# Optimization experiments

Hardware: AMD Instinct MI355X
Metric: run time of the kernel (lower is better)

## Reference

```python
import jax, jax.numpy as jnp
import numpy as np

B, LQ, LK, E, H = 2, 1024, 10000, 256, 8
D = E // H  # head_dim = 32


def setup_inputs() -> dict:
    key = jax.random.key(0)
    ks = jax.random.split(key, 10)
    s = 1.0 / np.sqrt(E).astype(np.float32)
    return {
        "bev_emb": jax.random.normal(ks[0], (B, LK, E), jnp.float32),
        "queries": jax.random.normal(ks[1], (B, LQ, E), jnp.float32),
        "Wq": jax.random.normal(ks[2], (E, E), jnp.float32) * s,
        "bq": jax.random.normal(ks[3], (E,), jnp.float32) * 0.01,
        "Wk": jax.random.normal(ks[4], (E, E), jnp.float32) * s,
        "bk": jax.random.normal(ks[5], (E,), jnp.float32) * 0.01,
        "Wv": jax.random.normal(ks[6], (E, E), jnp.float32) * s,
        "bv": jax.random.normal(ks[7], (E,), jnp.float32) * 0.01,
        "Wo": jax.random.normal(ks[8], (E, E), jnp.float32) * s,
        "bo": jax.random.normal(ks[9], (E,), jnp.float32) * 0.01,
    }


def reference(bev_emb, queries, Wq, bq, Wk, bk, Wv, bv, Wo, bo):
    Bn, Lq, Em = queries.shape
    Lk = bev_emb.shape[1]
    q = (queries @ Wq + bq).reshape(Bn, Lq, H, D)
    k = (bev_emb @ Wk + bk).reshape(Bn, Lk, H, D)
    v = (bev_emb @ Wv + bv).reshape(Bn, Lk, H, D)
    # NOTE: source applies no 1/sqrt(head_dim) scaling
    energy = jnp.einsum('bqhd,bkhd->bhqk', q, k)  # [B,H,Lq,Lk]
    attn = jax.nn.softmax(energy, axis=-1)
    out = jnp.einsum('bhqk,bkhd->bqhd', attn, v).reshape(Bn, Lq, Em)
    return out @ Wo + bo
```

## Files before the change

kernel.cpp:

```cpp
#include <hip/hip_runtime.h>
#include <hip/hip_bf16.h>

#define B_  2
#define LQ_ 1024
#define LK_ 10000
#define E_  256
#define H_  8
#define D_  32
#define NT_ ((LK_ + 63) / 64)
#define KVBLKS_ 625
#define QBLKS_  64

typedef __attribute__((ext_vector_type(8))) short bf16x8;
typedef __attribute__((ext_vector_type(4))) short bf16x4;
typedef __attribute__((ext_vector_type(4))) float f32x4;

#define LOG2E 1.4426950408889634f

static __device__ __forceinline__ short bfc(float x) {
  __bf16 b = (__bf16)x;
  return __builtin_bit_cast(short, b);
}
static __device__ __forceinline__ float bf2f(short s) {
  return (float)__builtin_bit_cast(__bf16, s);
}

#if __has_builtin(__builtin_amdgcn_exp2f)
static __device__ __forceinline__ float ex2(float x) {
  return __builtin_amdgcn_exp2f(x);
}
#else
static __device__ __forceinline__ float ex2(float x) { return exp2f(x); }
#endif

#if __has_builtin(__builtin_amdgcn_mfma_f32_16x16x16bf16_1k)
static __device__ __forceinline__ f32x4 mfma_pv(bf16x4 a, bf16x4 b, f32x4 c) {
  return __builtin_amdgcn_mfma_f32_16x16x16bf16_1k(a, b, c, 0, 0, 0);
}
#else
static __device__ __forceinline__ f32x4 mfma_pv(bf16x4 a, bf16x4 b, f32x4 c) {
  asm volatile("s_nop 1\n\tv_mfma_f32_16x16x16_bf16 %0, %1, %2, %0"
               : "+v"(c) : "v"(a), "v"(b));
  return c;
}
#endif

static __device__ __forceinline__ void tile_barrier() {
  __builtin_amdgcn_sched_barrier(0);
  asm volatile("s_waitcnt lgkmcnt(0)" ::: "memory");
  __builtin_amdgcn_s_barrier();
  __builtin_amdgcn_sched_barrier(0);
}

static __device__ __forceinline__ int xcd_swizzle(int flat, int nwg) {
  const int xcd = flat & 7, rest = flat >> 3;
  const int q = nwg >> 3, r = nwg & 7;
  return (xcd < r ? xcd * (q + 1) : r * (q + 1) + (xcd - r) * q) + rest;
}

static __device__ __forceinline__ void split8(const float4& a, const float4& b,
                                              bf16x8& hi, bf16x8& lo) {
  float v[8] = {a.x, a.y, a.z, a.w, b.x, b.y, b.z, b.w};
#pragma unroll
  for (int i = 0; i < 8; ++i) {
    const short h = bfc(v[i]);
    hi[i] = h;
    lo[i] = bfc(v[i] - bf2f(h));
  }
}

__global__ __launch_bounds__(256) void wtrans4(
    const float* __restrict__ W0, const float* __restrict__ W1,
    const float* __restrict__ W2, const float* __restrict__ W3,
    unsigned short* __restrict__ T0, unsigned short* __restrict__ T1,
    unsigned short* __restrict__ T2, unsigned short* __restrict__ T3) {
  const float* W;
  unsigned short* T;
  switch (blockIdx.z) {
    case 0:  W = W0; T = T0; break;
    case 1:  W = W1; T = T1; break;
    case 2:  W = W2; T = T2; break;
    default: W = W3; T = T3; break;
  }
  __shared__ float ts[16][17];
  const int tx = threadIdx.x & 15;
  const int ty = threadIdx.x >> 4;
  const int k0 = blockIdx.x * 16;
  const int n0 = blockIdx.y * 16;
  ts[ty][tx] = W[(size_t)(k0 + ty) * 256 + n0 + tx];
  __syncthreads();
  T[(size_t)(n0 + ty) * 256 + k0 + tx] = (unsigned short)bfc(ts[tx][ty]);
}

__global__ __launch_bounds__(256) void proj_all(
    const float* __restrict__ bev, const float* __restrict__ queries,
    const unsigned short* __restrict__ Wtk, const unsigned short* __restrict__ Wtv,
    const unsigned short* __restrict__ Wtq,
    const float* __restrict__ bk, const float* __restrict__ bv,
    const float* __restrict__ bq,
    unsigned short* __restrict__ kout, unsigned short* __restrict__ vout,
    float* __restrict__ qout) {
  const int lane = threadIdx.x & 63;
  const int nt   = threadIdx.x >> 6;
  const int lr   = lane & 15;
  const int oc   = lane >> 4;
  const int n0   = nt * 64;

  const bool isQ = (blockIdx.x >= KVBLKS_);
  const int  m0  = (isQ ? (int)blockIdx.x - KVBLKS_ : (int)blockIdx.x) * 32;
  const float* A = isQ ? queries : bev;
  const unsigned short* W1 = isQ ? Wtq : Wtk;

  f32x4 ac1[2][4], ac2[2][4];
#pragma unroll
  for (int s = 0; s < 2; ++s)
#pragma unroll
    for (int q = 0; q < 4; ++q) {
      ac1[s][q] = (f32x4){0.f, 0.f, 0.f, 0.f};
      ac2[s][q] = (f32x4){0.f, 0.f, 0.f, 0.f};
    }

  const float* a0p = &A[(size_t)(m0 + lr) * 256 + oc * 8];
  const float* a1p = a0p + 16 * 256;

  float4 ab[2][4];
  ab[0][0] = *(const float4*)(a0p + 0);
  ab[0][1] = *(const float4*)(a0p + 4);
  ab[0][2] = *(const float4*)(a1p + 0);
  ab[0][3] = *(const float4*)(a1p + 4);
  ab[1][0] = *(const float4*)(a0p + 32);
  ab[1][1] = *(const float4*)(a0p + 36);
  ab[1][2] = *(const float4*)(a1p + 32);
  ab[1][3] = *(const float4*)(a1p + 36);

#pragma unroll
  for (int kb = 0; kb < 8; ++kb) {
    const int bk_ = kb & 1;

    const int wko = kb * 32 + oc * 8;
    bf16x8 w1[4], w2[4];
#pragma unroll
    for (int q = 0; q < 4; ++q) {
      w1[q] = *(const bf16x8*)&W1[(size_t)(n0 + q * 16 + lr) * 256 + wko];
      if (!isQ) w2[q] = *(const bf16x8*)&Wtv[(size_t)(n0 + q * 16 + lr) * 256 + wko];
    }

    bf16x8 ah0, al0, ah1, al1;
    split8(ab[bk_][0], ab[bk_][1], ah0, al0);
    split8(ab[bk_][2], ab[bk_][3], ah1, al1);

    if (kb < 6) {
      ab[bk_][0] = *(const float4*)(a0p + (kb + 2) * 32 + 0);
      ab[bk_][1] = *(const float4*)(a0p + (kb + 2) * 32 + 4);
      ab[bk_][2] = *(const float4*)(a1p + (kb + 2) * 32 + 0);
      ab[bk_][3] = *(const float4*)(a1p + (kb + 2) * 32 + 4);
    }

#pragma unroll
    for (int q = 0; q < 4; ++q) {
      ac1[0][q] = __builtin_amdgcn_mfma_f32_16x16x32_bf16(w1[q], ah0, ac1[0][q], 0, 0, 0);
      ac1[0][q] = __builtin_amdgcn_mfma_f32_16x16x32_bf16(w1[q], al0, ac1[0][q], 0, 0, 0);
      ac1[1][q] = __builtin_amdgcn_mfma_f32_16x16x32_bf16(w1[q], ah1, ac1[1][q], 0, 0, 0);
      ac1[1][q] = __builtin_amdgcn_mfma_f32_16x16x32_bf16(w1[q], al1, ac1[1][q], 0, 0, 0);
      if (!isQ) {
        ac2[0][q] = __builtin_amdgcn_mfma_f32_16x16x32_bf16(w2[q], ah0, ac2[0][q], 0, 0, 0);
        ac2[1][q] = __builtin_amdgcn_mfma_f32_16x16x32_bf16(w2[q], ah1, ac2[1][q], 0, 0, 0);
      }
    }
  }

#pragma unroll
  for (int s = 0; s < 2; ++s) {
#pragma unroll
    for (int q = 0; q < 4; ++q) {
      const int m = m0 + s * 16 + lr;
      const int n = n0 + q * 16 + oc * 4;
      if (isQ) {
        const float4 b4 = *(const float4*)&bq[n];
        float4 o;
        o.x = ac1[s][q][0] + b4.x; o.y = ac1[s][q][1] + b4.y;
        o.z = ac1[s][q][2] + b4.z; o.w = ac1[s][q][3] + b4.w;
        *(float4*)&qout[(size_t)m * 256 + n] = o;
      } else {
        const float4 bk4 = *(const float4*)&bk[n];
        const float4 bv4 = *(const float4*)&bv[n];
        ushort4 ok, ov;
        ok.x = (unsigned short)bfc(ac1[s][q][0] + bk4.x);
        ok.y = (unsigned short)bfc(ac1[s][q][1] + bk4.y);
        ok.z = (unsigned short)bfc(ac1[s][q][2] + bk4.z);
        ok.w = (unsigned short)bfc(ac1[s][q][3] + bk4.w);
        ov.x = (unsigned short)bfc(ac2[s][q][0] + bv4.x);
        ov.y = (unsigned short)bfc(ac2[s][q][1] + bv4.y);
        ov.z = (unsigned short)bfc(ac2[s][q][2] + bv4.z);
        ov.w = (unsigned short)bfc(ac2[s][q][3] + bv4.w);
        *(ushort4*)&kout[(size_t)m * 256 + n] = ok;
        *(ushort4*)&vout[(size_t)m * 256 + n] = ov;
      }
    }
  }
}

__global__ __launch_bounds__(256) void proj_o(const float* __restrict__ A,
                                              const unsigned short* __restrict__ Wt,
                                              const float* __restrict__ bias,
                                              float* __restrict__ C) {
  const int lane = threadIdx.x & 63;
  const int nt   = threadIdx.x >> 6;
  const int lr   = lane & 15;
  const int oc   = lane >> 4;
  const int n0   = nt * 64;
  const int m0   = blockIdx.x * 32;

  f32x4 acc[2][4];
#pragma unroll
  for (int s = 0; s < 2; ++s)
#pragma unroll
    for (int q = 0; q < 4; ++q) acc[s][q] = (f32x4){0.f, 0.f, 0.f, 0.f};

  const float* a0p = &A[(size_t)(m0 + lr) * 256 + oc * 8];
  const float* a1p = a0p + 16 * 256;

  float4 ab[2][4];
  ab[0][0] = *(const float4*)(a0p + 0);
  ab[0][1] = *(const float4*)(a0p + 4);
  ab[0][2] = *(const float4*)(a1p + 0);
  ab[0][3] = *(const float4*)(a1p + 4);
  ab[1][0] = *(const float4*)(a0p + 32);
  ab[1][1] = *(const float4*)(a0p + 36);
  ab[1][2] = *(const float4*)(a1p + 32);
  ab[1][3] = *(const float4*)(a1p + 36);

#pragma unroll
  for (int kb = 0; kb < 8; ++kb) {
    const int bk_ = kb & 1;
    const int wko = kb * 32 + oc * 8;
    bf16x8 w[4];
#pragma unroll
    for (int q = 0; q < 4; ++q)
      w[q] = *(const bf16x8*)&Wt[(size_t)(n0 + q * 16 + lr) * 256 + wko];

    bf16x8 ah0, al0, ah1, al1;
    split8(ab[bk_][0], ab[bk_][1], ah0, al0);
    split8(ab[bk_][2], ab[bk_][3], ah1, al1);

    if (kb < 6) {
      ab[bk_][0] = *(const float4*)(a0p + (kb + 2) * 32 + 0);
      ab[bk_][1] = *(const float4*)(a0p + (kb + 2) * 32 + 4);
      ab[bk_][2] = *(const float4*)(a1p + (kb + 2) * 32 + 0);
      ab[bk_][3] = *(const float4*)(a1p + (kb + 2) * 32 + 4);
    }

#pragma unroll
    for (int q = 0; q < 4; ++q) {
      acc[0][q] = __builtin_amdgcn_mfma_f32_16x16x32_bf16(w[q], ah0, acc[0][q], 0, 0, 0);
      acc[0][q] = __builtin_amdgcn_mfma_f32_16x16x32_bf16(w[q], al0, acc[0][q], 0, 0, 0);
      acc[1][q] = __builtin_amdgcn_mfma_f32_16x16x32_bf16(w[q], ah1, acc[1][q], 0, 0, 0);
      acc[1][q] = __builtin_amdgcn_mfma_f32_16x16x32_bf16(w[q], al1, acc[1][q], 0, 0, 0);
    }
  }

#pragma unroll
  for (int s = 0; s < 2; ++s) {
#pragma unroll
    for (int q = 0; q < 4; ++q) {
      const int m = m0 + s * 16 + lr;
      const int n = n0 + q * 16 + oc * 4;
      const float4 b4 = *(const float4*)&bias[n];
      float4 o;
      o.x = acc[s][q][0] + b4.x; o.y = acc[s][q][1] + b4.y;
      o.z = acc[s][q][2] + b4.z; o.w = acc[s][q][3] + b4.w;
      *(float4*)&C[(size_t)m * 256 + n] = o;
    }
  }
}

__global__ __launch_bounds__(256, 4) void attn_mfma(const float* __restrict__ q,
                                                    const unsigned short* __restrict__ kbf,
                                                    const unsigned short* __restrict__ vbf,
                                                    float* __restrict__ Opart,
                                                    float* __restrict__ lpart,
                                                    float* __restrict__ o_direct,
                                                    int tiles_per_split, int nsplit) {
  const int nwg = 64 * gridDim.z;
  const int l   = xcd_swizzle(blockIdx.x + 8 * (blockIdx.y + 8 * blockIdx.z), nwg);
  const int qb   = l & 7;
  const int h    = (l >> 3) & 7;
  const int z    = l >> 6;
  const int s_id = z / B_;
  const int b    = z % B_;
  const int t    = threadIdx.x;
  const int lane = t & 63;
  const int w    = t >> 6;
  const int lq   = lane & 15;
  const int grp  = lane >> 4;

  __shared__ ushort Klds[2][64][64];
  __shared__ ushort Vtld[2][32][64];

  const int t0 = s_id * tiles_per_split;
  const int t1 = min(NT_, t0 + tiles_per_split);

  const int qrowA = qb * 128 + w * 32 + lq;
  const int qrowB = qrowA + 16;
  bf16x8 qfA, qfB;
  {
    const float* qpA = &q[((size_t)(b * LQ_ + qrowA)) * E_ + h * D_ + grp * 8];
    const float* qpB = &q[((size_t)(b * LQ_ + qrowB)) * E_ + h * D_ + grp * 8];
    const float4 a0 = *(const float4*)qpA;
    const float4 a1 = *(const float4*)(qpA + 4);
    const float4 b0 = *(const float4*)qpB;
    const float4 b1 = *(const float4*)(qpB + 4);
    qfA[0] = bfc(a0.x * LOG2E); qfA[1] = bfc(a0.y * LOG2E);
    qfA[2] = bfc(a0.z * LOG2E); qfA[3] = bfc(a0.w * LOG2E);
    qfA[4] = bfc(a1.x * LOG2E); qfA[5] = bfc(a1.y * LOG2E);
    qfA[6] = bfc(a1.z * LOG2E); qfA[7] = bfc(a1.w * LOG2E);
    qfB[0] = bfc(b0.x * LOG2E); qfB[1] = bfc(b0.y * LOG2E);
    qfB[2] = bfc(b0.z * LOG2E); qfB[3] = bfc(b0.w * LOG2E);
    qfB[4] = bfc(b1.x * LOG2E); qfB[5] = bfc(b1.y * LOG2E);
    qfB[6] = bfc(b1.z * LOG2E); qfB[7] = bfc(b1.w * LOG2E);
  }

  const int krow_l = t >> 2;
  const int kchunk = t & 3;
  const int vkp    = t >> 3;
  const int vd     = (t & 7) * 4;

  f32x4 lAv = {0.f, 0.f, 0.f, 0.f}, lBv = {0.f, 0.f, 0.f, 0.f};
  f32x4 a0A = {0.f, 0.f, 0.f, 0.f}, a1A = {0.f, 0.f, 0.f, 0.f};
  f32x4 a0B = {0.f, 0.f, 0.f, 0.f}, a1B = {0.f, 0.f, 0.f, 0.f};

  const size_t kvrow0 = (size_t)b * LK_;

  uint4 kval; ushort4 v0, v1;
  auto load_tile = [&](int kn) {
    if (kn == NT_ - 1) {
      const int krow  = min(kn * 64 + krow_l, LK_ - 1);
      const int vrow0 = min(kn * 64 + 2 * vkp, LK_ - 1);
      const int vrow1 = min(kn * 64 + 2 * vkp + 1, LK_ - 1);
      kval = *(const uint4*)&kbf[(kvrow0 + krow) * E_ + h * D_ + kchunk * 8];
      v0 = *(const ushort4*)&vbf[(kvrow0 + vrow0) * E_ + h * D_ + vd];
      v1 = *(const ushort4*)&vbf[(kvrow0 + vrow1) * E_ + h * D_ + vd];
    } else {
      kval = *(const uint4*)&kbf[(kvrow0 + kn * 64 + krow_l) * E_ + h * D_ + kchunk * 8];
      v0 = *(const ushort4*)&vbf[(kvrow0 + kn * 64 + 2 * vkp) * E_ + h * D_ + vd];
      v1 = *(const ushort4*)&vbf[(kvrow0 + kn * 64 + 2 * vkp + 1) * E_ + h * D_ + vd];
    }
  };
  auto store_tile = [&](int buf) {
    *(uint4*)((char*)&Klds[buf][krow_l][0] + ((kchunk * 16) ^ ((krow_l & 7) << 4))) = kval;
#pragma unroll
    for (int i = 0; i < 4; ++i) {
      const int d = vd + i;
      *(ushort2*)((char*)&Vtld[buf][d][0] + ((vkp * 4) ^ ((d & 7) << 4))) =
          make_ushort2(((const unsigned short*)&v0)[i], ((const unsigned short*)&v1)[i]);
    }
  };

  load_tile(t0);
  store_tile(0);
  if (t0 + 1 < t1) load_tile(t0 + 1);
  tile_barrier();

  int cur = 0;
  for (int kt = t0; kt < t1; ++kt) {
    const int rem = LK_ - kt * 64;

    if (kt + 1 < t1) store_tile(cur ^ 1);
    if (kt + 2 < t1) load_tile(kt + 2);

    f32x4 pA[4], pB[4];
    __builtin_amdgcn_s_setprio(1);
#pragma unroll
    for (int s = 0; s < 4; ++s) {
      const int row = s * 16 + lq;
      const bf16x8 kf = *(const bf16x8*)((const char*)&Klds[cur][row][0] +
                                         ((grp * 16) ^ ((row & 7) << 4)));
      const f32x4 zero = {0.f, 0.f, 0.f, 0.f};
      pA[s] = __builtin_amdgcn_mfma_f32_16x16x32_bf16(kf, qfA, zero, 0, 0, 0);
      pB[s] = __builtin_amdgcn_mfma_f32_16x16x32_bf16(kf, qfB, zero, 0, 0, 0);
    }
    __builtin_amdgcn_s_setprio(0);

    bf16x4 pbA[4], pbB[4];
    if (rem >= 64) {
#pragma unroll
      for (int s = 0; s < 4; ++s)
#pragma unroll
        for (int r = 0; r < 4; ++r) {
          const float eA = ex2(pA[s][r]);
          const float eB = ex2(pB[s][r]);
          lAv[r] += eA; lBv[r] += eB;
          pbA[s][r] = bfc(eA); pbB[s][r] = bfc(eB);
        }
    } else {
#pragma unroll
      for (int s = 0; s < 4; ++s) {
        const bool vs = (s * 16 + grp * 4) < rem;
#pragma unroll
        for (int r = 0; r < 4; ++r) {
          const float eA = vs ? ex2(pA[s][r]) : 0.f;
          const float eB = vs ? ex2(pB[s][r]) : 0.f;
          lAv[r] += eA; lBv[r] += eB;
          pbA[s][r] = bfc(eA); pbB[s][r] = bfc(eB);
        }
      }
    }

    __builtin_amdgcn_s_setprio(1);
#pragma unroll
    for (int s = 0; s < 4; ++s) {
      {
        const int row = lq;
        const bf16x4 vf = *(const bf16x4*)((const char*)&Vtld[cur][row][0] +
                                           ((s * 32 + grp * 8) ^ ((row & 7) << 4)));
        a0A = mfma_pv(vf, pbA[s], a0A);
        a0B = mfma_pv(vf, pbB[s], a0B);
      }
      {
        const int row = 16 + lq;
        const bf16x4 vf = *(const bf16x4*)((const char*)&Vtld[cur][row][0] +
                                           ((s * 32 + grp * 8) ^ ((row & 7) << 4)));
        a1A = mfma_pv(vf, pbA[s], a1A);
        a1B = mfma_pv(vf, pbB[s], a1B);
      }
    }
    __builtin_amdgcn_s_setprio(0);

    tile_barrier();
    cur ^= 1;
  }

  float lA = (lAv[0] + lAv[1]) + (lAv[2] + lAv[3]);
  float lB = (lBv[0] + lBv[1]) + (lBv[2] + lBv[3]);
  lA += __shfl_xor(lA, 16);
  lA += __shfl_xor(lA, 32);
  lB += __shfl_xor(lB, 16);
  lB += __shfl_xor(lB, 32);

  if (nsplit == 1) {
    const float invA = 1.f / lA;
    const float invB = 1.f / lB;
    float* opA = &o_direct[((size_t)(b * LQ_ + qrowA)) * E_ + h * D_];
    float* opB = &o_direct[((size_t)(b * LQ_ + qrowB)) * E_ + h * D_];
#pragma unroll
    for (int r = 0; r < 4; ++r) {
      opA[grp * 4 + r]      = a0A[r] * invA;
      opA[16 + grp * 4 + r] = a1A[r] * invA;
      opB[grp * 4 + r]      = a0B[r] * invB;
      opB[16 + grp * 4 + r] = a1B[r] * invB;
    }
  } else {
    const size_t pbA =
        (size_t)s_id * (B_ * H_ * LQ_) + ((size_t)b * H_ + h) * LQ_ + qrowA;
    const size_t pbB = pbA + 16;
#pragma unroll
    for (int r = 0; r < 4; ++r) {
      Opart[pbA * D_ + grp * 4 + r]      = a0A[r];
      Opart[pbA * D_ + 16 + grp * 4 + r] = a1A[r];
      Opart[pbB * D_ + grp * 4 + r]      = a0B[r];
      Opart[pbB * D_ + 16 + grp * 4 + r] = a1B[r];
    }
    if (grp == 0) {
      lpart[pbA] = lA;
      lpart[pbB] = lB;
    }
  }
}

__global__ __launch_bounds__(256) void attn_merge(const float* __restrict__ Opart,
                                                  const float* __restrict__ lpart,
                                                  float* __restrict__ o, int S) {
  const int idx = blockIdx.x * 256 + threadIdx.x;
  if (idx >= B_ * LQ_ * E_) return;
  const int e   = idx & (E_ - 1);
  const int row = idx >> 8;
  const int b   = row >> 10;
  const int qq  = row & (LQ_ - 1);
  const int h   = e >> 5;
  const int d   = e & (D_ - 1);
  const size_t base   = ((size_t)b * H_ + h) * LQ_ + qq;
  const size_t stride = (size_t)B_ * H_ * LQ_;

  float lsum = 0.f, osum = 0.f;
  for (int s = 0; s < S; ++s) {
    lsum += lpart[s * stride + base];
    osum += Opart[(s * stride + base) * D_ + d];
  }
  o[idx] = osum / lsum;
}

extern "C" void kernel_launch(void* const* d_in, const int* in_sizes, int n_in,
                              void* d_out, int out_size, void* d_ws, size_t ws_size,
                              hipStream_t stream) {
  const float* bev     = (const float*)d_in[0];
  const float* queries = (const float*)d_in[1];
  const float* Wq      = (const float*)d_in[2];
  const float* bq      = (const float*)d_in[3];
  const float* Wk      = (const float*)d_in[4];
  const float* bk      = (const float*)d_in[5];
  const float* Wv      = (const float*)d_in[6];
  const float* bv      = (const float*)d_in[7];
  const float* Wo      = (const float*)d_in[8];
  const float* bo      = (const float*)d_in[9];
  float* out = (float*)d_out;

  const size_t nq = (size_t)B_ * LQ_ * E_;
  const size_t nk = (size_t)B_ * LK_ * E_;
  const size_t nw = (size_t)E_ * E_;
  float*          qws = (float*)d_ws;
  unsigned short* kbf = (unsigned short*)(qws + nq);
  unsigned short* vbf = kbf + nk;
  float*          ows = (float*)(vbf + nk);
  unsigned short* Wtq = (unsigned short*)(ows + nq);
  unsigned short* Wtk = Wtq + nw;
  unsigned short* Wtv = Wtk + nw;
  unsigned short* Wto = Wtv + nw;
  float*          opart = (float*)(Wto + nw);

  const size_t base_bytes = (nq * 2) * sizeof(float) +
                            (nk * 2 + nw * 4) * sizeof(unsigned short);
  const size_t per_split_bytes = (size_t)B_ * H_ * LQ_ * (D_ + 1) * sizeof(float);
  const int cands[4] = {8, 4, 2, 1};
  int S = 1;
  for (int ci = 0; ci < 4; ++ci) {
    if (base_bytes + (size_t)cands[ci] * per_split_bytes <= ws_size) {
      S = cands[ci];
      break;
    }
  }

  wtrans4<<<dim3(16, 16, 4), 256, 0, stream>>>(Wq, Wk, Wv, Wo, Wtq, Wtk, Wtv, Wto);

  proj_all<<<dim3(KVBLKS_ + QBLKS_), 256, 0, stream>>>(
      bev, queries, Wtk, Wtv, Wtq, bk, bv, bq, kbf, vbf, qws);

  if (S <= 1) {
    attn_mfma<<<dim3(8, H_, B_), 256, 0, stream>>>(
        qws, kbf, vbf, nullptr, nullptr, ows, NT_, 1);
  } else {
    float* lpart = opart + (size_t)S * B_ * H_ * LQ_ * D_;
    const int tps = (NT_ + S - 1) / S;
    attn_mfma<<<dim3(8, H_, B_ * S), 256, 0, stream>>>(
        qws, kbf, vbf, opart, lpart, nullptr, tps, S);
    attn_merge<<<dim3((B_ * LQ_ * E_ + 255) / 256), 256, 0, stream>>>(
        opart, lpart, ows, S);
  }

  proj_o<<<dim3(QBLKS_), 256, 0, stream>>>(ows, Wto, bo, out);
}
```

Measured before the change: 109.3 us.

## Load K fragments straight from global into registers, bypassing LDS staging

K tiles are no longer staged through shared memory. Each lane loads its MFMA K fragments directly from global memory into registers, double-buffered across two register sets, with the loop unrolled by two so the buffers alternate. This removes the LDS writes and reads for K and shrinks LDS use, which could raise occupancy. In exchange it adds register pressure from eight extra bf16x8 registers, and each lane makes 16-byte global loads spread over more rows. An early return is added for splits that start past the last tile.

Result: slower. 177.7 us (+62.6%).

```diff
diff --git a/kernel.cpp b/kernel.cpp
--- a/kernel.cpp
+++ b/kernel.cpp
@@ -294,11 +294,11 @@
   const int lq   = lane & 15;
   const int grp  = lane >> 4;
 
-  __shared__ ushort Klds[2][64][64];
   __shared__ ushort Vtld[2][32][64];
 
   const int t0 = s_id * tiles_per_split;
   const int t1 = min(NT_, t0 + tiles_per_split);
+  if (t0 >= NT_) return;
 
   const int qrowA = qb * 128 + w * 32 + lq;
   const int qrowB = qrowA + 16;
@@ -320,10 +320,8 @@
     qfB[6] = bfc(b1.z * LOG2E); qfB[7] = bfc(b1.w * LOG2E);
   }
 
-  const int krow_l = t >> 2;
-  const int kchunk = t & 3;
-  const int vkp    = t >> 3;
-  const int vd     = (t & 7) * 4;
+  const int vkp = t >> 3;
+  const int vd  = (t & 7) * 4;
 
   f32x4 lAv = {0.f, 0.f, 0.f, 0.f}, lBv = {0.f, 0.f, 0.f, 0.f};
   f32x4 a0A = {0.f, 0.f, 0.f, 0.f}, a1A = {0.f, 0.f, 0.f, 0.f};
@@ -331,104 +329,107 @@
 
   const size_t kvrow0 = (size_t)b * LK_;
 
-  uint4 kval; ushort4 v0, v1;
-  auto load_tile = [&](int kn) {
-    if (kn == NT_ - 1) {
-      const int krow  = min(kn * 64 + krow_l, LK_ - 1);
-      const int vrow0 = min(kn * 64 + 2 * vkp, LK_ - 1);
-      const int vrow1 = min(kn * 64 + 2 * vkp + 1, LK_ - 1);
-      kval = *(const uint4*)&kbf[(kvrow0 + krow) * E_ + h * D_ + kchunk * 8];
-      v0 = *(const ushort4*)&vbf[(kvrow0 + vrow0) * E_ + h * D_ + vd];
-      v1 = *(const ushort4*)&vbf[(kvrow0 + vrow1) * E_ + h * D_ + vd];
-    } else {
-      kval = *(const uint4*)&kbf[(kvrow0 + kn * 64 + krow_l) * E_ + h * D_ + kchunk * 8];
-      v0 = *(const ushort4*)&vbf[(kvrow0 + kn * 64 + 2 * vkp) * E_ + h * D_ + vd];
-      v1 = *(const ushort4*)&vbf[(kvrow0 + kn * 64 + 2 * vkp + 1) * E_ + h * D_ + vd];
-    }
-  };
-  auto store_tile = [&](int buf) {
-    *(uint4*)((char*)&Klds[buf][krow_l][0] + ((kchunk * 16) ^ ((krow_l & 7) << 4))) = kval;
-#pragma unroll
-    for (int i = 0; i < 4; ++i) {
-      const int d = vd + i;
-      *(ushort2*)((char*)&Vtld[buf][d][0] + ((vkp * 4) ^ ((d & 7) << 4))) =
-          make_ushort2(((const unsigned short*)&v0)[i], ((const unsigned short*)&v1)[i]);
-    }
-  };
-
-  load_tile(t0);
-  store_tile(0);
-  if (t0 + 1 < t1) load_tile(t0 + 1);
+  ushort4 v0, v1;
+  bf16x8 kregA[4], kregB[4];
+
+#define LOADK_(KREG, KN)                                                       \
+  {                                                                            \
+    _Pragma("unroll") for (int s_ = 0; s_ < 4; ++s_) {                         \
+      const int row_ = min((KN) * 64 + s_ * 16 + lq, LK_ - 1);                 \
+      KREG[s_] = *(const bf16x8*)&kbf[(kvrow0 + row_) * E_ + h * D_ + grp * 8];\
+    }                                                                          \
+  }
+
+#define LOADV_(KN)                                                             \
+  {                                                                            \
+    const int vr0_ = min((KN) * 64 + 2 * vkp, LK_ - 1);                        \
+    const int vr1_ = min((KN) * 64 + 2 * vkp + 1, LK_ - 1);                    \
+    v0 = *(const ushort4*)&vbf[(kvrow0 + vr0_) * E_ + h * D_ + vd];            \
+    v1 = *(const ushort4*)&vbf[(kvrow0 + vr1_) * E_ + h * D_ + vd];            \
+  }
+
+#define STOREV_(BUF)                                                           \
+  {                                                                            \
+    _Pragma("unroll") for (int i_ = 0; i_ < 4; ++i_) {                         \
+      const int d_ = vd + i_;                                                  \
+      *(ushort2*)((char*)&Vtld[BUF][d_][0] + ((vkp * 4) ^ ((d_ & 7) << 4))) =  \
+          make_ushort2(((const unsigned short*)&v0)[i_],                       \
+                       ((const unsigned short*)&v1)[i_]);                      \
+    }                                                                          \
+  }
+
+#define BODY_(KREG, KT, CUR)                                                   \
+  {                                                                            \
+    const int rem_ = LK_ - (KT) * 64;                                          \
+    if ((KT) + 1 < t1) STOREV_((CUR) ^ 1);                                     \
+    if ((KT) + 2 < t1) LOADV_((KT) + 2);                                       \
+    f32x4 pA_[4], pB_[4];                                                      \
+    __builtin_amdgcn_s_setprio(1);                                             \
+    _Pragma("unroll") for (int s_ = 0; s_ < 4; ++s_) {                         \
+      const f32x4 z_ = {0.f, 0.f, 0.f, 0.f};                                   \
+      pA_[s_] = __builtin_amdgcn_mfma_f32_16x16x32_bf16(KREG[s_], qfA, z_, 0, 0, 0); \
+      pB_[s_] = __builtin_amdgcn_mfma_f32_16x16x32_bf16(KREG[s_], qfB, z_, 0, 0, 0); \
+    }                                                                          \
+    __builtin_amdgcn_s_setprio(0);                                             \
+    if ((KT) + 2 < t1) LOADK_(KREG, (KT) + 2);                                 \
+    bf16x4 pbA_[4], pbB_[4];                                                   \
+    if (rem_ >= 64) {                                                          \
+      _Pragma("unroll") for (int s_ = 0; s_ < 4; ++s_) {                       \
+        _Pragma("unroll") for (int r_ = 0; r_ < 4; ++r_) {                     \
+          const float eA_ = ex2(pA_[s_][r_]);                                  \
+          const float eB_ = ex2(pB_[s_][r_]);                                  \
+          lAv[r_] += eA_; lBv[r_] += eB_;                                      \
+          pbA_[s_][r_] = bfc(eA_); pbB_[s_][r_] = bfc(eB_);                    \
+        }                                                                      \
+      }                                                                        \
+    } else {                                                                   \
+      _Pragma("unroll") for (int s_ = 0; s_ < 4; ++s_) {                       \
+        const bool vs_ = (s_ * 16 + grp * 4) < rem_;                           \
+        _Pragma("unroll") for (int r_ = 0; r_ < 4; ++r_) {                     \
+          const float eA_ = vs_ ? ex2(pA_[s_][r_]) : 0.f;                      \
+          const float eB_ = vs_ ? ex2(pB_[s_][r_]) : 0.f;                      \
+          lAv[r_] += eA_; lBv[r_] += eB_;                                      \
+          pbA_[s_][r_] = bfc(eA_); pbB_[s_][r_] = bfc(eB_);                    \
+        }                                                                      \
+      }                                                                        \
+    }                                                                          \
+    __builtin_amdgcn_s_setprio(1);                                             \
+    _Pragma("unroll") for (int s_ = 0; s_ < 4; ++s_) {                         \
+      {                                                                        \
+        const bf16x4 vf_ = *(const bf16x4*)((const char*)&Vtld[CUR][lq][0] +   \
+                             ((s_ * 32 + grp * 8) ^ ((lq & 7) << 4)));         \
+        a0A = mfma_pv(vf_, pbA_[s_], a0A);                                     \
+        a0B = mfma_pv(vf_, pbB_[s_], a0B);                                     \
+      }                                                                        \
+      {                                                                        \
+        const bf16x4 vf_ = *(const bf16x4*)((const char*)&Vtld[CUR][16 + lq][0] + \
+                             ((s_ * 32 + grp * 8) ^ (((16 + lq) & 7) << 4)));  \
+        a1A = mfma_pv(vf_, pbA_[s_], a1A);                                     \
+        a1B = mfma_pv(vf_, pbB_[s_], a1B);                                     \
+      }                                                                        \
+    }                                                                          \
+    __builtin_amdgcn_s_setprio(0);                                             \
+    tile_barrier();                                                            \
+  }
+
+  LOADK_(kregA, t0);
+  LOADV_(t0);
+  STOREV_(0);
+  if (t0 + 1 < t1) {
+    LOADV_(t0 + 1);
+    LOADK_(kregB, t0 + 1);
+  }
   tile_barrier();
 
-  int cur = 0;
-  for (int kt = t0; kt < t1; ++kt) {
-    const int rem = LK_ - kt * 64;
-
-    if (kt + 1 < t1) store_tile(cur ^ 1);
-    if (kt + 2 < t1) load_tile(kt + 2);
-
-    f32x4 pA[4], pB[4];
-    __builtin_amdgcn_s_setprio(1);
-#pragma unroll
-    for (int s = 0; s < 4; ++s) {
-      const int row = s * 16 + lq;
-      const bf16x8 kf = *(const bf16x8*)((const char*)&Klds[cur][row][0] +
-                                         ((grp * 16) ^ ((row & 7) << 4)));
-      const f32x4 zero = {0.f, 0.f, 0.f, 0.f};
-      pA[s] = __builtin_amdgcn_mfma_f32_16x16x32_bf16(kf, qfA, zero, 0, 0, 0);
-      pB[s] = __builtin_amdgcn_mfma_f32_16x16x32_bf16(kf, qfB, zero, 0, 0, 0);
-    }
-    __builtin_amdgcn_s_setprio(0);
-
-    bf16x4 pbA[4], pbB[4];
-    if (rem >= 64) {
-#pragma unroll
-      for (int s = 0; s < 4; ++s)
-#pragma unroll
-        for (int r = 0; r < 4; ++r) {
-          const float eA = ex2(pA[s][r]);
-          const float eB = ex2(pB[s][r]);
-          lAv[r] += eA; lBv[r] += eB;
-          pbA[s][r] = bfc(eA); pbB[s][r] = bfc(eB);
-        }
-    } else {
-#pragma unroll
-      for (int s = 0; s < 4; ++s) {
-        const bool vs = (s * 16 + grp * 4) < rem;
-#pragma unroll
-        for (int r = 0; r < 4; ++r) {
-          const float eA = vs ? ex2(pA[s][r]) : 0.f;
-          const float eB = vs ? ex2(pB[s][r]) : 0.f;
-          lAv[r] += eA; lBv[r] += eB;
-          pbA[s][r] = bfc(eA); pbB[s][r] = bfc(eB);
-        }
-      }
-    }
-
-    __builtin_amdgcn_s_setprio(1);
-#pragma unroll
-    for (int s = 0; s < 4; ++s) {
-      {
-        const int row = lq;
-        const bf16x4 vf = *(const bf16x4*)((const char*)&Vtld[cur][row][0] +
-                                           ((s * 32 + grp * 8) ^ ((row & 7) << 4)));
-        a0A = mfma_pv(vf, pbA[s], a0A);
-        a0B = mfma_pv(vf, pbB[s], a0B);
-      }
-      {
-        const int row = 16 + lq;
-        const bf16x4 vf = *(const bf16x4*)((const char*)&Vtld[cur][row][0] +
-                                           ((s * 32 + grp * 8) ^ ((row & 7) << 4)));
-        a1A = mfma_pv(vf, pbA[s], a1A);
-        a1B = mfma_pv(vf, pbB[s], a1B);
-      }
-    }
-    __builtin_amdgcn_s_setprio(0);
-
-    tile_barrier();
-    cur ^= 1;
-  }
+  for (int kt = t0; kt < t1; kt += 2) {
+    BODY_(kregA, kt, 0);
+    if (kt + 1 < t1) BODY_(kregB, kt + 1, 1);
+  }
+
+#undef LOADK_
+#undef LOADV_
+#undef STOREV_
+#undef BODY_
 
   float lA = (lAv[0] + lAv[1]) + (lAv[2] + lAv[3]);
   float lB = (lBv[0] + lBv[1]) + (lBv[2] + lBv[3]);
```
